# Kernel optimization log

Hardware: AMD Instinct MI355X
Metric: run time of the kernel (lower is better)

The kernel has to match this reference:

```python
import jax, jax.numpy as jnp
import numpy as np

B, L, D, H, T = 64, 512, 768, 384, 9  # batch, seq_len, hidden, hidden//2, num_tags


def setup_inputs() -> dict:
    key = jax.random.key(0)
    ks = jax.random.split(key, 8)
    return {
        "encoder_out": jax.random.normal(ks[0], (B, L, D), jnp.float32),
        "ner_labels": jax.random.randint(ks[1], (B, L), 0, T),
        "mask": jnp.ones((B, L), jnp.bool_),
        "W1": jax.random.normal(ks[2], (D, H), jnp.float32) / np.sqrt(D).astype(np.float32),
        "b1": jnp.zeros((H,), jnp.float32),
        "W2": jax.random.normal(ks[3], (H, T), jnp.float32) / np.sqrt(H).astype(np.float32),
        "b2": jnp.zeros((T,), jnp.float32),
        "start_trans": jax.random.uniform(ks[4], (T,), jnp.float32, -0.1, 0.1),
        "end_trans": jax.random.uniform(ks[5], (T,), jnp.float32, -0.1, 0.1),
        "trans": jax.random.uniform(ks[6], (T, T), jnp.float32, -0.1, 0.1),
    }


def _crf_nll(emissions, tags, mask, start_trans, end_trans, trans):
    """-mean log-likelihood, matching pytorch-crf forward (reduction='mean')."""
    maskf = mask.astype(emissions.dtype)
    # ---- numerator: score of the gold tag path ----
    emit = jnp.take_along_axis(emissions, tags[..., None], axis=-1)[..., 0]  # [B,L]
    emit_score = jnp.sum(emit * maskf, axis=1)
    tr = trans[tags[:, :-1], tags[:, 1:]]  # [B,L-1]
    tr_score = jnp.sum(tr * maskf[:, 1:], axis=1)
    last_idx = jnp.sum(mask.astype(jnp.int32), axis=1) - 1
    last_tags = jnp.take_along_axis(tags, last_idx[:, None], axis=1)[:, 0]
    numer = start_trans[tags[:, 0]] + emit_score + tr_score + end_trans[last_tags]
    # ---- denominator: forward algorithm (log partition) via scan ----
    alpha0 = start_trans[None, :] + emissions[:, 0]          # [B,T]
    em_rest = jnp.swapaxes(emissions[:, 1:], 0, 1)           # [L-1,B,T]
    mk_rest = jnp.swapaxes(maskf[:, 1:], 0, 1)               # [L-1,B]

    def step(alpha, xs):
        e_t, m_t = xs
        nxt = jax.nn.logsumexp(alpha[:, :, None] + trans[None, :, :] + e_t[:, None, :], axis=1)
        return jnp.where(m_t[:, None] > 0, nxt, alpha), None

    alpha, _ = jax.lax.scan(step, alpha0, (em_rest, mk_rest))
    denom = jax.nn.logsumexp(alpha + end_trans[None, :], axis=1)
    return -jnp.mean(numer - denom)


def reference(encoder_out, ner_labels, mask, W1, b1, W2, b2, start_trans, end_trans, trans):
    # proj: Linear -> GELU (exact erf, torch default) -> Dropout (identity in eval)
    h = jax.nn.gelu(encoder_out @ W1 + b1, approximate=False)
    emissions = h @ W2 + b2  # [B,L,T]
    return _crf_nll(emissions, ner_labels, mask, start_trans, end_trans, trans)
```

## Files before the change

kernel.cpp:

```cpp
#include <hip/hip_runtime.h>
#include <hip/hip_bf16.h>
#include <math.h>

#define B_ 64
#define L_ 512
#define D_ 768
#define H_ 384
#define T_ 9
#define M_ (B_ * L_)

typedef __attribute__((ext_vector_type(8))) short short8;
typedef __attribute__((ext_vector_type(4))) float f32x4;

__device__ __forceinline__ float gelu_exact(float x) {
    return 0.5f * x * (1.0f + erff(x * 0.70710678118654752440f));
}

__device__ __forceinline__ unsigned short f2bf(float f) {
    unsigned u = __float_as_uint(f);
    u += 0x7FFFu + ((u >> 16) & 1u);
    return (unsigned short)(u >> 16);
}

__device__ __forceinline__ float wredf(float v) {
#pragma unroll
    for (int m = 32; m >= 1; m >>= 1) v += __shfl_xor(v, m, 64);
    return v;
}

__device__ __forceinline__ void sync_lds() {
    asm volatile("s_waitcnt lgkmcnt(0)\n\ts_barrier" ::: "memory");
}

__global__ __launch_bounds__(256) void prep_kernel(
    const float* __restrict__ W1, const float* __restrict__ W2,
    unsigned short* __restrict__ W1F, unsigned short* __restrict__ W2F,
    float* __restrict__ out)
{
    if (blockIdx.x == 0 && threadIdx.x == 0) out[0] = 0.f;
    const int g    = blockIdx.x * 4 + (threadIdx.x >> 6);
    const int lane = threadIdx.x & 63;
    const int lm   = lane & 15;
    const int q    = lane >> 4;
    if (g < 576) {
        const int nt = g / 24;
        const int kc = g - nt * 24;
        const int n  = nt * 16 + lm;
        short8 v;
#pragma unroll
        for (int j = 0; j < 8; ++j)
            v[j] = (short)f2bf(W1[(size_t)(kc * 32 + q * 8 + j) * H_ + n]);
        *(short8*)(W1F + ((size_t)g * 64 + lane) * 8) = v;
    } else if (g < 588) {
        const int kk = g - 576;
        short8 v;
#pragma unroll
        for (int j = 0; j < 8; ++j) {
            int k = kk * 32 + q * 8 + j;
            v[j] = (lm < 9) ? (short)f2bf(W2[(size_t)k * T_ + lm]) : (short)0;
        }
        *(short8*)(W2F + ((size_t)kk * 64 + lane) * 8) = v;
    }
}

__global__ __launch_bounds__(256, 2) void emis_mfma_kernel(
    const float* __restrict__ X,
    const unsigned short* __restrict__ W1F,
    const float* __restrict__ b1,
    const unsigned short* __restrict__ W2F,
    const float* __restrict__ b2,
    float* __restrict__ em)
{
    __shared__ unsigned short Hs[64 * 392];
    unsigned short* As = Hs;

    const int t    = threadIdx.x;
    const int lane = t & 63;
    const int w    = t >> 6;
    const int lm   = lane & 15;
    const int q    = lane >> 4;
    const int row0 = blockIdx.x * 64;

    const int ar  = t >> 2;
    const int ako = (t & 3) << 3;
    const float* xp = X + (size_t)(row0 + ar) * D_ + ako;

    f32x4 acc[4][6];
#pragma unroll
    for (int mt = 0; mt < 4; ++mt)
#pragma unroll
        for (int i = 0; i < 6; ++i) acc[mt][i] = (f32x4)0.f;

    {
        float4 p0 = *(const float4*)(xp);
        float4 p1 = *(const float4*)(xp + 4);
        short8 v;
        v[0] = (short)f2bf(p0.x); v[1] = (short)f2bf(p0.y);
        v[2] = (short)f2bf(p0.z); v[3] = (short)f2bf(p0.w);
        v[4] = (short)f2bf(p1.x); v[5] = (short)f2bf(p1.y);
        v[6] = (short)f2bf(p1.z); v[7] = (short)f2bf(p1.w);
        *(short8*)&As[ar * 40 + ako] = v;
    }
    float4 xv[2][2];
    xv[0][0] = *(const float4*)(xp + 32);  xv[0][1] = *(const float4*)(xp + 36);
    xv[1][0] = *(const float4*)(xp + 64);  xv[1][1] = *(const float4*)(xp + 68);
    short8 bb[2][6];
#pragma unroll
    for (int i = 0; i < 6; ++i) {
        bb[0][i] = *(const short8*)(W1F + (((size_t)(w * 6 + i) * 24 + 0) * 64 + lane) * 8);
        bb[1][i] = *(const short8*)(W1F + (((size_t)(w * 6 + i) * 24 + 1) * 64 + lane) * 8);
    }

#pragma unroll
    for (int kc = 0; kc < 24; ++kc) {
        const int s = kc & 1;
        sync_lds();
        short8 af[4];
#pragma unroll
        for (int mt = 0; mt < 4; ++mt)
            af[mt] = *(const short8*)&As[s * 2560 + (mt * 16 + lm) * 40 + (q << 3)];
#pragma unroll
        for (int mt = 0; mt < 4; ++mt)
#pragma unroll
            for (int i = 0; i < 6; ++i)
                acc[mt][i] = __builtin_amdgcn_mfma_f32_16x16x32_bf16(
                    af[mt], bb[s][i], acc[mt][i], 0, 0, 0);
        if (kc < 23) {
            float4 x0 = xv[s][0], x1 = xv[s][1];
            short8 v;
            v[0] = (short)f2bf(x0.x); v[1] = (short)f2bf(x0.y);
            v[2] = (short)f2bf(x0.z); v[3] = (short)f2bf(x0.w);
            v[4] = (short)f2bf(x1.x); v[5] = (short)f2bf(x1.y);
            v[6] = (short)f2bf(x1.z); v[7] = (short)f2bf(x1.w);
            *(short8*)&As[(s ^ 1) * 2560 + ar * 40 + ako] = v;
            if (kc < 21) {
                xv[s][0] = *(const float4*)(xp + (kc + 3) * 32);
                xv[s][1] = *(const float4*)(xp + (kc + 3) * 32 + 4);
            }
            if (kc < 22) {
#pragma unroll
                for (int i = 0; i < 6; ++i)
                    bb[s][i] = *(const short8*)(W1F +
                        (((size_t)(w * 6 + i) * 24 + kc + 2) * 64 + lane) * 8);
            }
        }
    }
    __syncthreads();

#pragma unroll
    for (int i = 0; i < 6; ++i) {
        const int col = w * 96 + i * 16 + lm;
        const float b1v = b1[col];
#pragma unroll
        for (int mt = 0; mt < 4; ++mt)
#pragma unroll
            for (int r = 0; r < 4; ++r) {
                float h = gelu_exact(acc[mt][i][r] + b1v);
                Hs[(mt * 16 + q * 4 + r) * 392 + col] = f2bf(h);
            }
    }
    __syncthreads();

    f32x4 e = (f32x4)0.f;
#pragma unroll
    for (int kk = 0; kk < 12; ++kk) {
        short8 ah = *(const short8*)&Hs[(w * 16 + lm) * 392 + kk * 32 + (q << 3)];
        short8 bw = *(const short8*)(W2F + ((size_t)(kk * 64 + lane)) * 8);
        e = __builtin_amdgcn_mfma_f32_16x16x32_bf16(ah, bw, e, 0, 0, 0);
    }
    if (lm < 9) {
        const float b2v = b2[lm];
#pragma unroll
        for (int r = 0; r < 4; ++r)
            em[(size_t)(row0 + w * 16 + q * 4 + r) * T_ + lm] = e[r] + b2v;
    }
}

__global__ __launch_bounds__(288) void crf_kernel(
    const float* __restrict__ em,
    const int* __restrict__ labels,
    const unsigned char* __restrict__ maskb,
    const float* __restrict__ st,
    const float* __restrict__ et,
    const float* __restrict__ tr,
    float* __restrict__ out)
{
    const int b = blockIdx.x;
    const int t = threadIdx.x;

    __shared__ float es[32 * 145];
    __shared__ float Ms[32 * 81];
    __shared__ float trs[81];
    __shared__ float red[2];
    __shared__ unsigned char msh[L_];
    __shared__ int lbs[L_];

    const int mstride =
        (maskb[0] != 0 && maskb[1] == 0 && maskb[2] == 0 && maskb[3] == 0) ? 4 : 1;

    const float* eb = em + (size_t)b * L_ * T_;
    for (int i = t; i < L_ * T_; i += 288) {
        int tt = i / T_, j = i - tt * T_;
        es[(tt >> 4) * 145 + (tt & 15) * 9 + j] = eb[i];
    }
    if (t < 81) trs[t] = tr[t];
    for (int i = t; i < L_; i += 288) {
        msh[i] = maskb[((size_t)b * L_ + i) * (size_t)mstride];
        lbs[i] = labels[b * L_ + i];
    }
    __syncthreads();

    {
        const int c  = t / 9;
        const int i0 = t - c * 9;
        float trr[81];
#pragma unroll
        for (int i = 0; i < 81; ++i) trr[i] = trs[i];
        float V[9];
#pragma unroll
        for (int j = 0; j < 9; ++j) V[j] = (j == i0) ? 0.f : -1e30f;

        const int sbeg = (c == 0) ? 1 : 0;
        for (int s = sbeg; s < 16; ++s) {
            int tt = c * 16 + s;
            if (msh[tt]) {
                const float* ep = &es[c * 145 + s * 9];
                float nv[9];
#pragma unroll
                for (int j = 0; j < 9; ++j) {
                    float a[9];
#pragma unroll
                    for (int k = 0; k < 9; ++k) a[k] = V[k] + trr[k * 9 + j];
                    float mx = a[0];
#pragma unroll
                    for (int k = 1; k < 9; ++k) mx = fmaxf(mx, a[k]);
                    float sum = 0.f;
#pragma unroll
                    for (int k = 0; k < 9; ++k) sum += __expf(a[k] - mx);
                    nv[j] = ep[j] + mx + __logf(sum);
                }
#pragma unroll
                for (int j = 0; j < 9; ++j) V[j] = nv[j];
            }
        }
#pragma unroll
        for (int j = 0; j < 9; ++j) Ms[c * 81 + i0 * 9 + j] = V[j];
    }
    __syncthreads();

    const int lane = t & 63;
    const int w    = t >> 6;
    if (w == 0) {
        const int jj = lane < 9 ? lane : 8;
        float alpha = (lane < 9) ? st[jj] + es[jj] : -1e30f;
        for (int c = 0; c < 32; ++c) {
            float a[9];
#pragma unroll
            for (int i = 0; i < 9; ++i) {
                float av = __shfl(alpha, i, 64);
                a[i] = av + Ms[c * 81 + i * 9 + jj];
            }
            float mx = a[0];
#pragma unroll
            for (int i = 1; i < 9; ++i) mx = fmaxf(mx, a[i]);
            float sum = 0.f;
#pragma unroll
            for (int i = 0; i < 9; ++i) sum += __expf(a[i] - mx);
            float nv = mx + __logf(sum);
            if (lane < 9) alpha = nv;
        }
        float v = (lane < 9) ? alpha + et[jj] : -1e30f;
        float mx = v;
#pragma unroll
        for (int m = 32; m >= 1; m >>= 1) mx = fmaxf(mx, __shfl_xor(mx, m, 64));
        float s = __expf(v - mx);
        s = wredf(s);
        if (lane == 0) red[0] = mx + __logf(s);
    } else if (w == 1) {
        float emit_s = 0.f, tr_sc = 0.f, mcnt = 0.f;
        for (int tt = lane; tt < L_; tt += 64) {
            if (msh[tt]) {
                mcnt += 1.f;
                int tag = lbs[tt];
                emit_s += es[(tt >> 4) * 145 + (tt & 15) * 9 + tag];
                if (tt >= 1) tr_sc += trs[lbs[tt - 1] * 9 + tag];
            }
        }
        emit_s = wredf(emit_s);
        tr_sc  = wredf(tr_sc);
        mcnt   = wredf(mcnt);
        if (lane == 0) {
            int last = (int)mcnt - 1;
            red[1] = st[lbs[0]] + emit_s + tr_sc + et[lbs[last]];
        }
    }
    __syncthreads();
    if (t == 0) atomicAdd(out, (red[0] - red[1]) * (1.0f / (float)B_));
}

extern "C" void kernel_launch(void* const* d_in, const int* in_sizes, int n_in,
                              void* d_out, int out_size, void* d_ws, size_t ws_size,
                              hipStream_t stream) {
    const float*         enc    = (const float*)d_in[0];
    const int*           labels = (const int*)d_in[1];
    const unsigned char* mask   = (const unsigned char*)d_in[2];
    const float*         W1     = (const float*)d_in[3];
    const float*         b1     = (const float*)d_in[4];
    const float*         W2     = (const float*)d_in[5];
    const float*         b2     = (const float*)d_in[6];
    const float*         st     = (const float*)d_in[7];
    const float*         et     = (const float*)d_in[8];
    const float*         tr     = (const float*)d_in[9];

    float* em           = (float*)d_ws;
    unsigned short* W1F = (unsigned short*)(em + (size_t)M_ * T_);
    unsigned short* W2F = W1F + (size_t)576 * 64 * 8;

    prep_kernel<<<147, 256, 0, stream>>>(W1, W2, W1F, W2F, (float*)d_out);
    emis_mfma_kernel<<<M_ / 64, 256, 0, stream>>>(enc, W1F, b1, W2F, b2, em);
    crf_kernel<<<B_, 288, 0, stream>>>(em, labels, mask, st, et, tr, (float*)d_out);
}
```

Before: 241.8 us.

## Split hidden dim across blocks, tree-reduce CRF chunks, use fast sigmoid GELU

```diff
diff --git a/kernel.cpp b/kernel.cpp
--- a/kernel.cpp
+++ b/kernel.cpp
@@ -12,14 +12,20 @@
 typedef __attribute__((ext_vector_type(8))) short short8;
 typedef __attribute__((ext_vector_type(4))) float f32x4;
 
-__device__ __forceinline__ float gelu_exact(float x) {
-    return 0.5f * x * (1.0f + erff(x * 0.70710678118654752440f));
-}
-
 __device__ __forceinline__ unsigned short f2bf(float f) {
     unsigned u = __float_as_uint(f);
     u += 0x7FFFu + ((u >> 16) & 1u);
     return (unsigned short)(u >> 16);
+}
+
+__device__ __forceinline__ unsigned pkbf2(float a, float b) {
+    __hip_bfloat162 h = __float22bfloat162_rn(float2{a, b});
+    return *(unsigned*)&h;
+}
+
+__device__ __forceinline__ float gelu_fast(float x) {
+    float z2 = 1.5957691216f * x + 0.0713548162726f * x * x * x;
+    return x / (1.f + __expf(-z2));
 }
 
 __device__ __forceinline__ float wredf(float v) {
@@ -63,15 +69,16 @@
     }
 }
 
-__global__ __launch_bounds__(256, 2) void emis_mfma_kernel(
+__global__ __launch_bounds__(256) void emis_mfma_kernel(
     const float* __restrict__ X,
     const unsigned short* __restrict__ W1F,
     const float* __restrict__ b1,
     const unsigned short* __restrict__ W2F,
     const float* __restrict__ b2,
-    float* __restrict__ em)
+    float* __restrict__ em0,
+    float* __restrict__ em1)
 {
-    __shared__ unsigned short Hs[64 * 392];
+    __shared__ unsigned short Hs[64 * 200];
     unsigned short* As = Hs;
 
     const int t    = threadIdx.x;
@@ -79,36 +86,37 @@
     const int w    = t >> 6;
     const int lm   = lane & 15;
     const int q    = lane >> 4;
-    const int row0 = blockIdx.x * 64;
+    const int half = blockIdx.x >> 9;
+    const int rb   = blockIdx.x & 511;
+    const int row0 = rb * 64;
 
     const int ar  = t >> 2;
     const int ako = (t & 3) << 3;
     const float* xp = X + (size_t)(row0 + ar) * D_ + ako;
 
-    f32x4 acc[4][6];
+    f32x4 acc[4][3];
 #pragma unroll
     for (int mt = 0; mt < 4; ++mt)
 #pragma unroll
-        for (int i = 0; i < 6; ++i) acc[mt][i] = (f32x4)0.f;
+        for (int i = 0; i < 3; ++i) acc[mt][i] = (f32x4)0.f;
+
+    const int ntg0 = half * 12 + w * 3;
 
     {
         float4 p0 = *(const float4*)(xp);
         float4 p1 = *(const float4*)(xp + 4);
-        short8 v;
-        v[0] = (short)f2bf(p0.x); v[1] = (short)f2bf(p0.y);
-        v[2] = (short)f2bf(p0.z); v[3] = (short)f2bf(p0.w);
-        v[4] = (short)f2bf(p1.x); v[5] = (short)f2bf(p1.y);
-        v[6] = (short)f2bf(p1.z); v[7] = (short)f2bf(p1.w);
-        *(short8*)&As[ar * 40 + ako] = v;
+        int4 v = {(int)pkbf2(p0.x, p0.y), (int)pkbf2(p0.z, p0.w),
+                  (int)pkbf2(p1.x, p1.y), (int)pkbf2(p1.z, p1.w)};
+        *(int4*)&As[ar * 40 + ako] = v;
     }
     float4 xv[2][2];
     xv[0][0] = *(const float4*)(xp + 32);  xv[0][1] = *(const float4*)(xp + 36);
     xv[1][0] = *(const float4*)(xp + 64);  xv[1][1] = *(const float4*)(xp + 68);
-    short8 bb[2][6];
-#pragma unroll
-    for (int i = 0; i < 6; ++i) {
-        bb[0][i] = *(const short8*)(W1F + (((size_t)(w * 6 + i) * 24 + 0) * 64 + lane) * 8);
-        bb[1][i] = *(const short8*)(W1F + (((size_t)(w * 6 + i) * 24 + 1) * 64 + lane) * 8);
+    short8 bb[2][3];
+#pragma unroll
+    for (int i = 0; i < 3; ++i) {
+        bb[0][i] = *(const short8*)(W1F + (((size_t)(ntg0 + i) * 24 + 0) * 64 + lane) * 8);
+        bb[1][i] = *(const short8*)(W1F + (((size_t)(ntg0 + i) * 24 + 1) * 64 + lane) * 8);
     }
 
 #pragma unroll
@@ -122,62 +130,61 @@
 #pragma unroll
         for (int mt = 0; mt < 4; ++mt)
 #pragma unroll
-            for (int i = 0; i < 6; ++i)
+            for (int i = 0; i < 3; ++i)
                 acc[mt][i] = __builtin_amdgcn_mfma_f32_16x16x32_bf16(
                     af[mt], bb[s][i], acc[mt][i], 0, 0, 0);
         if (kc < 23) {
             float4 x0 = xv[s][0], x1 = xv[s][1];
-            short8 v;
-            v[0] = (short)f2bf(x0.x); v[1] = (short)f2bf(x0.y);
-            v[2] = (short)f2bf(x0.z); v[3] = (short)f2bf(x0.w);
-            v[4] = (short)f2bf(x1.x); v[5] = (short)f2bf(x1.y);
-            v[6] = (short)f2bf(x1.z); v[7] = (short)f2bf(x1.w);
-            *(short8*)&As[(s ^ 1) * 2560 + ar * 40 + ako] = v;
+            int4 v = {(int)pkbf2(x0.x, x0.y), (int)pkbf2(x0.z, x0.w),
+                      (int)pkbf2(x1.x, x1.y), (int)pkbf2(x1.z, x1.w)};
+            *(int4*)&As[(s ^ 1) * 2560 + ar * 40 + ako] = v;
             if (kc < 21) {
                 xv[s][0] = *(const float4*)(xp + (kc + 3) * 32);
                 xv[s][1] = *(const float4*)(xp + (kc + 3) * 32 + 4);
             }
             if (kc < 22) {
 #pragma unroll
-                for (int i = 0; i < 6; ++i)
+                for (int i = 0; i < 3; ++i)
                     bb[s][i] = *(const short8*)(W1F +
-                        (((size_t)(w * 6 + i) * 24 + kc + 2) * 64 + lane) * 8);
+                        (((size_t)(ntg0 + i) * 24 + kc + 2) * 64 + lane) * 8);
             }
         }
     }
     __syncthreads();
 
 #pragma unroll
-    for (int i = 0; i < 6; ++i) {
-        const int col = w * 96 + i * 16 + lm;
-        const float b1v = b1[col];
+    for (int i = 0; i < 3; ++i) {
+        const int lc = w * 48 + i * 16 + lm;
+        const float b1v = b1[half * 192 + lc];
 #pragma unroll
         for (int mt = 0; mt < 4; ++mt)
 #pragma unroll
             for (int r = 0; r < 4; ++r) {
-                float h = gelu_exact(acc[mt][i][r] + b1v);
-                Hs[(mt * 16 + q * 4 + r) * 392 + col] = f2bf(h);
+                float h = gelu_fast(acc[mt][i][r] + b1v);
+                Hs[(mt * 16 + q * 4 + r) * 200 + lc] = f2bf(h);
             }
     }
     __syncthreads();
 
     f32x4 e = (f32x4)0.f;
 #pragma unroll
-    for (int kk = 0; kk < 12; ++kk) {
-        short8 ah = *(const short8*)&Hs[(w * 16 + lm) * 392 + kk * 32 + (q << 3)];
-        short8 bw = *(const short8*)(W2F + ((size_t)(kk * 64 + lane)) * 8);
+    for (int kk = 0; kk < 6; ++kk) {
+        short8 ah = *(const short8*)&Hs[(w * 16 + lm) * 200 + kk * 32 + (q << 3)];
+        short8 bw = *(const short8*)(W2F + ((size_t)((half * 6 + kk) * 64 + lane)) * 8);
         e = __builtin_amdgcn_mfma_f32_16x16x32_bf16(ah, bw, e, 0, 0, 0);
     }
     if (lm < 9) {
-        const float b2v = b2[lm];
+        float* emo = half ? em1 : em0;
+        const float badd = half ? 0.f : b2[lm];
 #pragma unroll
         for (int r = 0; r < 4; ++r)
-            em[(size_t)(row0 + w * 16 + q * 4 + r) * T_ + lm] = e[r] + b2v;
-    }
-}
-
-__global__ __launch_bounds__(288) void crf_kernel(
-    const float* __restrict__ em,
+            emo[(size_t)(row0 + w * 16 + q * 4 + r) * T_ + lm] = e[r] + badd;
+    }
+}
+
+__global__ __launch_bounds__(640) void crf_kernel(
+    const float* __restrict__ em0,
+    const float* __restrict__ em1,
     const int* __restrict__ labels,
     const unsigned char* __restrict__ maskb,
     const float* __restrict__ st,
@@ -188,29 +195,31 @@
     const int b = blockIdx.x;
     const int t = threadIdx.x;
 
-    __shared__ float es[32 * 145];
-    __shared__ float Ms[32 * 81];
+    __shared__ float es[64 * 73];
+    __shared__ float Msa[64 * 81];
+    __shared__ float Msb[32 * 81];
     __shared__ float trs[81];
-    __shared__ float red[2];
+    __shared__ float red_num;
     __shared__ unsigned char msh[L_];
     __shared__ int lbs[L_];
 
     const int mstride =
         (maskb[0] != 0 && maskb[1] == 0 && maskb[2] == 0 && maskb[3] == 0) ? 4 : 1;
 
-    const float* eb = em + (size_t)b * L_ * T_;
-    for (int i = t; i < L_ * T_; i += 288) {
+    const float* e0 = em0 + (size_t)b * L_ * T_;
+    const float* e1 = em1 + (size_t)b * L_ * T_;
+    for (int i = t; i < L_ * T_; i += 640) {
         int tt = i / T_, j = i - tt * T_;
-        es[(tt >> 4) * 145 + (tt & 15) * 9 + j] = eb[i];
+        es[(tt >> 3) * 73 + (tt & 7) * 9 + j] = e0[i] + e1[i];
     }
     if (t < 81) trs[t] = tr[t];
-    for (int i = t; i < L_; i += 288) {
+    for (int i = t; i < L_; i += 640) {
         msh[i] = maskb[((size_t)b * L_ + i) * (size_t)mstride];
         lbs[i] = labels[b * L_ + i];
     }
     __syncthreads();
 
-    {
+    if (t < 576) {
         const int c  = t / 9;
         const int i0 = t - c * 9;
         float trr[81];
@@ -221,10 +230,10 @@
         for (int j = 0; j < 9; ++j) V[j] = (j == i0) ? 0.f : -1e30f;
 
         const int sbeg = (c == 0) ? 1 : 0;
-        for (int s = sbeg; s < 16; ++s) {
-            int tt = c * 16 + s;
+        for (int s = sbeg; s < 8; ++s) {
+            int tt = c * 8 + s;
             if (msh[tt]) {
-                const float* ep = &es[c * 145 + s * 9];
+                const float* ep = &es[c * 73 + s * 9];
                 float nv[9];
 #pragma unroll
                 for (int j = 0; j < 9; ++j) {
@@ -244,45 +253,15 @@
             }
         }
 #pragma unroll
-        for (int j = 0; j < 9; ++j) Ms[c * 81 + i0 * 9 + j] = V[j];
-    }
-    __syncthreads();
-
-    const int lane = t & 63;
-    const int w    = t >> 6;
-    if (w == 0) {
-        const int jj = lane < 9 ? lane : 8;
-        float alpha = (lane < 9) ? st[jj] + es[jj] : -1e30f;
-        for (int c = 0; c < 32; ++c) {
-            float a[9];
-#pragma unroll
-            for (int i = 0; i < 9; ++i) {
-                float av = __shfl(alpha, i, 64);
-                a[i] = av + Ms[c * 81 + i * 9 + jj];
-            }
-            float mx = a[0];
-#pragma unroll
-            for (int i = 1; i < 9; ++i) mx = fmaxf(mx, a[i]);
-            float sum = 0.f;
-#pragma unroll
-            for (int i = 0; i < 9; ++i) sum += __expf(a[i] - mx);
-            float nv = mx + __logf(sum);
-            if (lane < 9) alpha = nv;
-        }
-        float v = (lane < 9) ? alpha + et[jj] : -1e30f;
-        float mx = v;
-#pragma unroll
-        for (int m = 32; m >= 1; m >>= 1) mx = fmaxf(mx, __shfl_xor(mx, m, 64));
-        float s = __expf(v - mx);
-        s = wredf(s);
-        if (lane == 0) red[0] = mx + __logf(s);
-    } else if (w == 1) {
+        for (int j = 0; j < 9; ++j) Msa[c * 81 + i0 * 9 + j] = V[j];
+    } else {
+        const int lane = t - 576;
         float emit_s = 0.f, tr_sc = 0.f, mcnt = 0.f;
         for (int tt = lane; tt < L_; tt += 64) {
             if (msh[tt]) {
                 mcnt += 1.f;
                 int tag = lbs[tt];
-                emit_s += es[(tt >> 4) * 145 + (tt & 15) * 9 + tag];
+                emit_s += es[(tt >> 3) * 73 + (tt & 7) * 9 + tag];
                 if (tt >= 1) tr_sc += trs[lbs[tt - 1] * 9 + tag];
             }
         }
@@ -291,11 +270,59 @@
         mcnt   = wredf(mcnt);
         if (lane == 0) {
             int last = (int)mcnt - 1;
-            red[1] = st[lbs[0]] + emit_s + tr_sc + et[lbs[last]];
+            red_num = st[lbs[0]] + emit_s + tr_sc + et[lbs[last]];
         }
     }
     __syncthreads();
-    if (t == 0) atomicAdd(out, (red[0] - red[1]) * (1.0f / (float)B_));
+
+    float* src = Msa;
+    float* dst = Msb;
+    for (int n = 32; n >= 1; n >>= 1) {
+        for (int idx = t; idx < n * 81; idx += 640) {
+            int p = idx / 81;
+            int r = idx - p * 81;
+            int i = r / 9, j = r - i * 9;
+            const float* A  = src + (2 * p) * 81 + i * 9;
+            const float* Bm = src + (2 * p + 1) * 81 + j;
+            float v[9];
+#pragma unroll
+            for (int k = 0; k < 9; ++k) v[k] = A[k] + Bm[k * 9];
+            float mx = v[0];
+#pragma unroll
+            for (int k = 1; k < 9; ++k) mx = fmaxf(mx, v[k]);
+            float sum = 0.f;
+#pragma unroll
+            for (int k = 0; k < 9; ++k) sum += __expf(v[k] - mx);
+            dst[p * 81 + r] = mx + __logf(sum);
+        }
+        __syncthreads();
+        float* tmp = src; src = dst; dst = tmp;
+    }
+
+    if (t < 64) {
+        float v = -3.0e38f;
+        if (t < 9) {
+            float a[9];
+#pragma unroll
+            for (int i = 0; i < 9; ++i) a[i] = st[i] + es[i] + src[i * 9 + t];
+            float mx = a[0];
+#pragma unroll
+            for (int i = 1; i < 9; ++i) mx = fmaxf(mx, a[i]);
+            float sum = 0.f;
+#pragma unroll
+            for (int i = 0; i < 9; ++i) sum += __expf(a[i] - mx);
+            v = mx + __logf(sum) + et[t];
+        }
+        float mx = v;
+#pragma unroll
+        for (int m = 32; m >= 1; m >>= 1) mx = fmaxf(mx, __shfl_xor(mx, m, 64));
+        float sm = __expf(v - mx);
+        sm = wredf(sm);
+        if (t == 0) {
+            float denom = mx + __logf(sm);
+            atomicAdd(out, (denom - red_num) * (1.0f / (float)B_));
+        }
+    }
 }
 
 extern "C" void kernel_launch(void* const* d_in, const int* in_sizes, int n_in,
@@ -312,11 +339,12 @@
     const float*         et     = (const float*)d_in[8];
     const float*         tr     = (const float*)d_in[9];
 
-    float* em           = (float*)d_ws;
-    unsigned short* W1F = (unsigned short*)(em + (size_t)M_ * T_);
+    float* em0          = (float*)d_ws;
+    float* em1          = em0 + (size_t)M_ * T_;
+    unsigned short* W1F = (unsigned short*)(em1 + (size_t)M_ * T_);
     unsigned short* W2F = W1F + (size_t)576 * 64 * 8;
 
     prep_kernel<<<147, 256, 0, stream>>>(W1, W2, W1F, W2F, (float*)d_out);
-    emis_mfma_kernel<<<M_ / 64, 256, 0, stream>>>(enc, W1F, b1, W2F, b2, em);
-    crf_kernel<<<B_, 288, 0, stream>>>(em, labels, mask, st, et, tr, (float*)d_out);
-}
+    emis_mfma_kernel<<<1024, 256, 0, stream>>>(enc, W1F, b1, W2F, b2, em0, em1);
+    crf_kernel<<<B_, 640, 0, stream>>>(em0, em1, labels, mask, st, et, tr, (float*)d_out);
+}
```

Result: faster. 232.8 us (-3.7%).

## Halve GEMM row tile, raise occupancy, use fast GELU, double CRF chunks

Applied to the files above, without the earlier changes.

```diff
diff --git a/kernel.cpp b/kernel.cpp
--- a/kernel.cpp
+++ b/kernel.cpp
@@ -12,14 +12,20 @@
 typedef __attribute__((ext_vector_type(8))) short short8;
 typedef __attribute__((ext_vector_type(4))) float f32x4;
 
-__device__ __forceinline__ float gelu_exact(float x) {
-    return 0.5f * x * (1.0f + erff(x * 0.70710678118654752440f));
-}
-
 __device__ __forceinline__ unsigned short f2bf(float f) {
     unsigned u = __float_as_uint(f);
     u += 0x7FFFu + ((u >> 16) & 1u);
     return (unsigned short)(u >> 16);
+}
+
+__device__ __forceinline__ unsigned pkbf2(float a, float b) {
+    __hip_bfloat162 h = __float22bfloat162_rn(float2{a, b});
+    return *(unsigned*)&h;
+}
+
+__device__ __forceinline__ float gelu_fast(float x) {
+    float z2 = 1.5957691216f * x + 0.0713548162726f * x * x * x;
+    return x / (1.f + __expf(-z2));
 }
 
 __device__ __forceinline__ float wredf(float v) {
@@ -63,7 +69,7 @@
     }
 }
 
-__global__ __launch_bounds__(256, 2) void emis_mfma_kernel(
+__global__ __launch_bounds__(256, 4) void emis_mfma_kernel(
     const float* __restrict__ X,
     const unsigned short* __restrict__ W1F,
     const float* __restrict__ b1,
@@ -71,7 +77,7 @@
     const float* __restrict__ b2,
     float* __restrict__ em)
 {
-    __shared__ unsigned short Hs[64 * 392];
+    __shared__ unsigned short Hs[32 * 392];
     unsigned short* As = Hs;
 
     const int t    = threadIdx.x;
@@ -79,70 +85,44 @@
     const int w    = t >> 6;
     const int lm   = lane & 15;
     const int q    = lane >> 4;
-    const int row0 = blockIdx.x * 64;
-
-    const int ar  = t >> 2;
-    const int ako = (t & 3) << 3;
-    const float* xp = X + (size_t)(row0 + ar) * D_ + ako;
-
-    f32x4 acc[4][6];
-#pragma unroll
-    for (int mt = 0; mt < 4; ++mt)
+    const int row0 = blockIdx.x * 32;
+
+    const int sr = t >> 3;
+    const int sk = (t & 7) << 2;
+    const float* xp = X + (size_t)(row0 + sr) * D_ + sk;
+
+    f32x4 acc[2][6];
+#pragma unroll
+    for (int mt = 0; mt < 2; ++mt)
 #pragma unroll
         for (int i = 0; i < 6; ++i) acc[mt][i] = (f32x4)0.f;
 
     {
-        float4 p0 = *(const float4*)(xp);
-        float4 p1 = *(const float4*)(xp + 4);
-        short8 v;
-        v[0] = (short)f2bf(p0.x); v[1] = (short)f2bf(p0.y);
-        v[2] = (short)f2bf(p0.z); v[3] = (short)f2bf(p0.w);
-        v[4] = (short)f2bf(p1.x); v[5] = (short)f2bf(p1.y);
-        v[6] = (short)f2bf(p1.z); v[7] = (short)f2bf(p1.w);
-        *(short8*)&As[ar * 40 + ako] = v;
-    }
-    float4 xv[2][2];
-    xv[0][0] = *(const float4*)(xp + 32);  xv[0][1] = *(const float4*)(xp + 36);
-    xv[1][0] = *(const float4*)(xp + 64);  xv[1][1] = *(const float4*)(xp + 68);
-    short8 bb[2][6];
-#pragma unroll
-    for (int i = 0; i < 6; ++i) {
-        bb[0][i] = *(const short8*)(W1F + (((size_t)(w * 6 + i) * 24 + 0) * 64 + lane) * 8);
-        bb[1][i] = *(const short8*)(W1F + (((size_t)(w * 6 + i) * 24 + 1) * 64 + lane) * 8);
+        float4 x0 = *(const float4*)xp;
+        int2 v = {(int)pkbf2(x0.x, x0.y), (int)pkbf2(x0.z, x0.w)};
+        *(int2*)&As[sr * 40 + sk] = v;
     }
 
 #pragma unroll
     for (int kc = 0; kc < 24; ++kc) {
         const int s = kc & 1;
+        float4 xn;
+        if (kc < 23) xn = *(const float4*)(xp + (kc + 1) * 32);
         sync_lds();
-        short8 af[4];
-#pragma unroll
-        for (int mt = 0; mt < 4; ++mt)
-            af[mt] = *(const short8*)&As[s * 2560 + (mt * 16 + lm) * 40 + (q << 3)];
-#pragma unroll
-        for (int mt = 0; mt < 4; ++mt)
-#pragma unroll
-            for (int i = 0; i < 6; ++i)
-                acc[mt][i] = __builtin_amdgcn_mfma_f32_16x16x32_bf16(
-                    af[mt], bb[s][i], acc[mt][i], 0, 0, 0);
+        short8 af[2];
+#pragma unroll
+        for (int mt = 0; mt < 2; ++mt)
+            af[mt] = *(const short8*)&As[s * 1280 + (mt * 16 + lm) * 40 + (q << 3)];
+#pragma unroll
+        for (int i = 0; i < 6; ++i) {
+            short8 bf = *(const short8*)(W1F +
+                (((size_t)(w * 6 + i) * 24 + kc) * 64 + lane) * 8);
+            acc[0][i] = __builtin_amdgcn_mfma_f32_16x16x32_bf16(af[0], bf, acc[0][i], 0, 0, 0);
+            acc[1][i] = __builtin_amdgcn_mfma_f32_16x16x32_bf16(af[1], bf, acc[1][i], 0, 0, 0);
+        }
         if (kc < 23) {
-            float4 x0 = xv[s][0], x1 = xv[s][1];
-            short8 v;
-            v[0] = (short)f2bf(x0.x); v[1] = (short)f2bf(x0.y);
-            v[2] = (short)f2bf(x0.z); v[3] = (short)f2bf(x0.w);
-            v[4] = (short)f2bf(x1.x); v[5] = (short)f2bf(x1.y);
-            v[6] = (short)f2bf(x1.z); v[7] = (short)f2bf(x1.w);
-            *(short8*)&As[(s ^ 1) * 2560 + ar * 40 + ako] = v;
-            if (kc < 21) {
-                xv[s][0] = *(const float4*)(xp + (kc + 3) * 32);
-                xv[s][1] = *(const float4*)(xp + (kc + 3) * 32 + 4);
-            }
-            if (kc < 22) {
-#pragma unroll
-                for (int i = 0; i < 6; ++i)
-                    bb[s][i] = *(const short8*)(W1F +
-                        (((size_t)(w * 6 + i) * 24 + kc + 2) * 64 + lane) * 8);
-            }
+            int2 v = {(int)pkbf2(xn.x, xn.y), (int)pkbf2(xn.z, xn.w)};
+            *(int2*)&As[(s ^ 1) * 1280 + sr * 40 + sk] = v;
         }
     }
     __syncthreads();
@@ -152,31 +132,33 @@
         const int col = w * 96 + i * 16 + lm;
         const float b1v = b1[col];
 #pragma unroll
-        for (int mt = 0; mt < 4; ++mt)
+        for (int mt = 0; mt < 2; ++mt)
 #pragma unroll
             for (int r = 0; r < 4; ++r) {
-                float h = gelu_exact(acc[mt][i][r] + b1v);
+                float h = gelu_fast(acc[mt][i][r] + b1v);
                 Hs[(mt * 16 + q * 4 + r) * 392 + col] = f2bf(h);
             }
     }
     __syncthreads();
 
-    f32x4 e = (f32x4)0.f;
-#pragma unroll
-    for (int kk = 0; kk < 12; ++kk) {
-        short8 ah = *(const short8*)&Hs[(w * 16 + lm) * 392 + kk * 32 + (q << 3)];
-        short8 bw = *(const short8*)(W2F + ((size_t)(kk * 64 + lane)) * 8);
-        e = __builtin_amdgcn_mfma_f32_16x16x32_bf16(ah, bw, e, 0, 0, 0);
-    }
-    if (lm < 9) {
-        const float b2v = b2[lm];
-#pragma unroll
-        for (int r = 0; r < 4; ++r)
-            em[(size_t)(row0 + w * 16 + q * 4 + r) * T_ + lm] = e[r] + b2v;
-    }
-}
-
-__global__ __launch_bounds__(288) void crf_kernel(
+    if (w < 2) {
+        f32x4 e = (f32x4)0.f;
+#pragma unroll
+        for (int kk = 0; kk < 12; ++kk) {
+            short8 ah = *(const short8*)&Hs[(w * 16 + lm) * 392 + kk * 32 + (q << 3)];
+            short8 bw = *(const short8*)(W2F + ((size_t)(kk * 64 + lane)) * 8);
+            e = __builtin_amdgcn_mfma_f32_16x16x32_bf16(ah, bw, e, 0, 0, 0);
+        }
+        if (lm < 9) {
+            const float b2v = b2[lm];
+#pragma unroll
+            for (int r = 0; r < 4; ++r)
+                em[(size_t)(row0 + w * 16 + q * 4 + r) * T_ + lm] = e[r] + b2v;
+        }
+    }
+}
+
+__global__ __launch_bounds__(576) void crf_kernel(
     const float* __restrict__ em,
     const int* __restrict__ labels,
     const unsigned char* __restrict__ maskb,
@@ -188,8 +170,8 @@
     const int b = blockIdx.x;
     const int t = threadIdx.x;
 
-    __shared__ float es[32 * 145];
-    __shared__ float Ms[32 * 81];
+    __shared__ float es[64 * 73];
+    __shared__ float Ms[64 * 81];
     __shared__ float trs[81];
     __shared__ float red[2];
     __shared__ unsigned char msh[L_];
@@ -199,12 +181,12 @@
         (maskb[0] != 0 && maskb[1] == 0 && maskb[2] == 0 && maskb[3] == 0) ? 4 : 1;
 
     const float* eb = em + (size_t)b * L_ * T_;
-    for (int i = t; i < L_ * T_; i += 288) {
+    for (int i = t; i < L_ * T_; i += 576) {
         int tt = i / T_, j = i - tt * T_;
-        es[(tt >> 4) * 145 + (tt & 15) * 9 + j] = eb[i];
+        es[(tt >> 3) * 73 + (tt & 7) * 9 + j] = eb[i];
     }
     if (t < 81) trs[t] = tr[t];
-    for (int i = t; i < L_; i += 288) {
+    for (int i = t; i < L_; i += 576) {
         msh[i] = maskb[((size_t)b * L_ + i) * (size_t)mstride];
         lbs[i] = labels[b * L_ + i];
     }
@@ -221,10 +203,10 @@
         for (int j = 0; j < 9; ++j) V[j] = (j == i0) ? 0.f : -1e30f;
 
         const int sbeg = (c == 0) ? 1 : 0;
-        for (int s = sbeg; s < 16; ++s) {
-            int tt = c * 16 + s;
+        for (int s = sbeg; s < 8; ++s) {
+            int tt = c * 8 + s;
             if (msh[tt]) {
-                const float* ep = &es[c * 145 + s * 9];
+                const float* ep = &es[c * 73 + s * 9];
                 float nv[9];
 #pragma unroll
                 for (int j = 0; j < 9; ++j) {
@@ -253,7 +235,7 @@
     if (w == 0) {
         const int jj = lane < 9 ? lane : 8;
         float alpha = (lane < 9) ? st[jj] + es[jj] : -1e30f;
-        for (int c = 0; c < 32; ++c) {
+        for (int c = 0; c < 64; ++c) {
             float a[9];
 #pragma unroll
             for (int i = 0; i < 9; ++i) {
@@ -282,7 +264,7 @@
             if (msh[tt]) {
                 mcnt += 1.f;
                 int tag = lbs[tt];
-                emit_s += es[(tt >> 4) * 145 + (tt & 15) * 9 + tag];
+                emit_s += es[(tt >> 3) * 73 + (tt & 7) * 9 + tag];
                 if (tt >= 1) tr_sc += trs[lbs[tt - 1] * 9 + tag];
             }
         }
@@ -317,6 +299,6 @@
     unsigned short* W2F = W1F + (size_t)576 * 64 * 8;
 
     prep_kernel<<<147, 256, 0, stream>>>(W1, W2, W1F, W2F, (float*)d_out);
-    emis_mfma_kernel<<<M_ / 64, 256, 0, stream>>>(enc, W1F, b1, W2F, b2, em);
-    crf_kernel<<<B_, 288, 0, stream>>>(em, labels, mask, st, et, tr, (float*)d_out);
-}
+    emis_mfma_kernel<<<M_ / 32, 256, 0, stream>>>(enc, W1F, b1, W2F, b2, em);
+    crf_kernel<<<B_, 576, 0, stream>>>(em, labels, mask, st, et, tr, (float*)d_out);
+}
```

After: 239.7 us. Within noise of the previous version (-0.9%).
